# Performance work log

Hardware: AMD Instinct MI355X
Metric: run time of the kernel (lower is better)

The kernel has to match this reference:

```python
import jax, jax.numpy as jnp
import numpy as np

EXPANSION_RATES = [10, 25]
NEG_SLOPE = 0.2


def gat_layer(x_self, x_neigh, W, a_self, a_neigh):
    """Multi-head GAT attention over a fixed neighbor fanout.

    x_self:  [M, F]      target-node features
    x_neigh: [M, K, F]   K sampled neighbors per target
    W:       [H, F, D]   per-head projection
    a_self:  [H, D]      attention vector (self part)
    a_neigh: [H, D]      attention vector (neighbor part)
    returns  [M, H*D]    concatenated heads
    """
    hs = jnp.einsum('mf,hfd->mhd', x_self, W)              # [M,H,D]
    hn = jnp.einsum('mkf,hfd->mkhd', x_neigh, W)           # [M,K,H,D]
    e_self = jnp.einsum('mhd,hd->mh', hs, a_self)          # [M,H]
    e_neigh = jnp.einsum('mkhd,hd->mkh', hn, a_neigh)      # [M,K,H]
    e = jax.nn.leaky_relu(e_self[:, None, :] + e_neigh, NEG_SLOPE)
    alpha = jax.nn.softmax(e, axis=1)                      # softmax over K neighbors
    out = jnp.einsum('mkh,mkhd->mhd', alpha, hn)           # [M,H,D]
    return out.reshape(out.shape[0], -1)                   # concat heads


def setup_inputs() -> dict:
    key = jax.random.key(0)
    ks = jax.random.split(key, 10)
    B, F, D, H, OUT = 1024, 128, 128, 2, 128
    r0, r1 = EXPANSION_RATES
    inp = {}
    # hierarchical embeddings: level j has B * prod(rates[:j]) rows
    inp['h0'] = jax.random.normal(ks[0], (B, F), dtype=jnp.float32)
    inp['h1'] = jax.random.normal(ks[1], (B * r0, F), dtype=jnp.float32)
    inp['h2'] = jax.random.normal(ks[2], (B * r0 * r1, F), dtype=jnp.float32)
    # layer 0: consumes raw features (F); layer 1: consumes H*D
    inp['W0'] = jax.random.normal(ks[3], (H, F, D), dtype=jnp.float32) / np.sqrt(F)
    inp['a_self0'] = jax.random.normal(ks[4], (H, D), dtype=jnp.float32) / np.sqrt(D)
    inp['a_neigh0'] = jax.random.normal(ks[5], (H, D), dtype=jnp.float32) / np.sqrt(D)
    inp['W1'] = jax.random.normal(ks[6], (H, H * D, D), dtype=jnp.float32) / np.sqrt(H * D)
    inp['a_self1'] = jax.random.normal(ks[7], (H, D), dtype=jnp.float32) / np.sqrt(D)
    inp['a_neigh1'] = jax.random.normal(ks[8], (H, D), dtype=jnp.float32) / np.sqrt(D)
    inp['fc_W'] = jax.random.normal(ks[9], (H * D, OUT), dtype=jnp.float32) / np.sqrt(H * D)
    return inp


def reference(h0, h1, h2, W0, a_self0, a_neigh0, W1, a_self1, a_neigh1, fc_W):
    hidden = [h0, h1, h2]
    layers = [(W0, a_self0, a_neigh0), (W1, a_self1, a_neigh1)]
    depth = len(EXPANSION_RATES)
    for i, (W, a_s, a_n) in enumerate(layers):
        for j in range(depth - i):
            x_self = hidden[j]                                   # [M, F_i]
            M = x_self.shape[0]
            # neighbor rows of level j+1 grouped in blocks of expansion_rates[j]
            x_neigh = hidden[j + 1].reshape(M, EXPANSION_RATES[j], x_self.shape[1])
            hidden[j] = gat_layer(x_self, x_neigh, W, a_s, a_n)  # [M, H*D]
    return hidden[0] @ fc_W                                      # [B, OUT]
```

## Files before the change

### kernel.cpp

```cpp
#include <hip/hip_runtime.h>

#define LRELU_SLOPE 0.2f

#define OFF_UV0  0u
#define OFF_U1   512u
#define OFF_V1   1024u
#define OFF_P    1536u
#define OFF_PP   2048u
#define OFF_Q    4096u
#define OFF_R    69632u
#define OFF_Y1   135168u
#define OFF_Y0   2756608u

__device__ __forceinline__ float dot4(float4 a, float4 b) {
    return a.x * b.x + a.y * b.y + a.z * b.z + a.w * b.w;
}

template<int CTRL>
__device__ __forceinline__ float dppmov(float x) {
    return __int_as_float(__builtin_amdgcn_update_dpp(
        0, __float_as_int(x), CTRL, 0xf, 0xf, true));
}
__device__ __forceinline__ float sum16(float x) {
    x += dppmov<0xB1>(x);
    x += dppmov<0x4E>(x);
    x += dppmov<0x141>(x);
    x += dppmov<0x140>(x);
    return x;
}
__device__ __forceinline__ float sum32(float x) {
    x = sum16(x);
    return x + __shfl_xor(x, 16);
}
__device__ __forceinline__ float sum64(float x) {
    float y = sum32(x);
    return y + __shfl_xor(y, 32);
}
__device__ __forceinline__ float lrelu(float x) {
    return (x >= 0.f) ? x : LRELU_SLOPE * x;
}

__global__ __launch_bounds__(256)
void prepA_kernel(const float* __restrict__ W0, const float* __restrict__ as0,
                  const float* __restrict__ an0,
                  const float* __restrict__ W1, const float* __restrict__ as1,
                  const float* __restrict__ an1,
                  const float* __restrict__ fcW, float* __restrict__ ws) {
    __shared__ float s[16 * 129];
    const int b = blockIdx.x;
    const int t = threadIdx.x;
    if (b < 192) {
        const int wid = b * 4 + (t >> 6);
        const int lane = t & 63;
        const float *wrow, *as, *an;
        if (wid < 256) {
            wrow = W0 + (size_t)wid * 128;
            int h = wid >> 7;
            as = as0 + h * 128; an = an0 + h * 128;
        } else {
            int g = wid - 256;
            wrow = W1 + (size_t)g * 128;
            int h = g >> 8;
            as = as1 + h * 128; an = an1 + h * 128;
        }
        float2 w = *(const float2*)(wrow + 2 * lane);
        float2 sv = *(const float2*)(as + 2 * lane);
        float2 nv = *(const float2*)(an + 2 * lane);
        float au = sum64(w.x * sv.x + w.y * sv.y);
        float av = sum64(w.x * nv.x + w.y * nv.y);
        if (lane == 0) {
            if (wid < 256) { ws[OFF_UV0 + wid] = au; ws[OFF_UV0 + 256 + wid] = av; }
            else { int g = wid - 256; ws[OFF_U1 + g] = au; ws[OFF_V1 + g] = av; }
        }
    } else {
        const int idx = b - 192;
        const int h = idx >> 4, g0 = (idx & 15) * 16;
        const float* Wh = W1 + (size_t)h * 32768;
        for (int ii = t * 4; ii < 16 * 128; ii += 1024) {
            int i = ii >> 7, d = ii & 127;
            float4 g4 = *(const float4*)(Wh + (size_t)(g0 + i) * 128 + d);
            s[i * 129 + d + 0] = g4.x;
            s[i * 129 + d + 1] = g4.y;
            s[i * 129 + d + 2] = g4.z;
            s[i * 129 + d + 3] = g4.w;
        }
        __syncthreads();
        const int dg = t & 31, rg = t >> 5;
        float4 acc[2];
        acc[0] = make_float4(0.f, 0.f, 0.f, 0.f);
        acc[1] = make_float4(0.f, 0.f, 0.f, 0.f);
        const float* fp = fcW + (size_t)h * 16384 + 4 * dg;
        #pragma unroll 4
        for (int d2 = 0; d2 < 128; ++d2) {
            float4 f4 = *(const float4*)(fp + (size_t)d2 * 128);
            #pragma unroll
            for (int j = 0; j < 2; ++j) {
                float x = s[(rg * 2 + j) * 129 + d2];
                acc[j].x += x * f4.x; acc[j].y += x * f4.y;
                acc[j].z += x * f4.z; acc[j].w += x * f4.w;
            }
        }
        float* Qp = ws + OFF_Q + (size_t)h * 32768;
        #pragma unroll
        for (int j = 0; j < 2; ++j)
            *(float4*)(Qp + (size_t)(g0 + rg * 2 + j) * 128 + 4 * dg) = acc[j];
    }
}

__device__ __forceinline__ void upd2(float& m, float& s, float4& A,
                                     float ea, float eb,
                                     const float4& xa, const float4& xb) {
    float mn = fmaxf(m, fmaxf(ea, eb));
    float sc = __expf(m - mn);
    float pa = __expf(ea - mn);
    float pb = __expf(eb - mn);
    s = s * sc + pa + pb;
    A.x = A.x * sc + pa * xa.x + pb * xb.x;
    A.y = A.y * sc + pa * xa.y + pb * xb.y;
    A.z = A.z * sc + pa * xa.z + pb * xb.z;
    A.w = A.w * sc + pa * xa.w + pb * xb.w;
    m = mn;
}
__device__ __forceinline__ void upd1(float& m, float& s, float4& A,
                                     float ea, const float4& xa) {
    float mn = fmaxf(m, ea);
    float sc = __expf(m - mn);
    float pa = __expf(ea - mn);
    s = s * sc + pa;
    A.x = A.x * sc + pa * xa.x;
    A.y = A.y * sc + pa * xa.y;
    A.z = A.z * sc + pa * xa.z;
    A.w = A.w * sc + pa * xa.w;
    m = mn;
}

__global__ __launch_bounds__(256)
void big6_kernel(const float* __restrict__ h0, const float* __restrict__ h1,
                 const float* __restrict__ h2, const float* __restrict__ W0,
                 float* __restrict__ ws) {
    const int b = blockIdx.x;
    const int t = threadIdx.x;
    const float* uv0 = ws + OFF_UV0;

    if (b < 1280) {
        const int lane = t & 63;
        const int sub = lane >> 5;
        const int fl = lane & 31;
        const int m = (b * 4 + (t >> 6)) * 2 + sub;
        const float* xnp = h2 + (size_t)m * 3200;
        float es0, es1;
        {
            const float4 xs = *(const float4*)(h1 + (size_t)m * 128 + 4 * fl);
            const float4 u0 = *(const float4*)(uv0 + 0 + 4 * fl);
            const float4 u1 = *(const float4*)(uv0 + 128 + 4 * fl);
            es0 = sum32(dot4(xs, u0));
            es1 = sum32(dot4(xs, u1));
        }
        const float4 v0 = *(const float4*)(uv0 + 256 + 4 * fl);
        const float4 v1 = *(const float4*)(uv0 + 384 + 4 * fl);

        float4 xa = *(const float4*)(xnp + 4 * fl);
        float4 xb = *(const float4*)(xnp + 128 + 4 * fl);
        float4 xc = *(const float4*)(xnp + 256 + 4 * fl);
        float4 xd = *(const float4*)(xnp + 384 + 4 * fl);
        float m0 = -1e30f, m1 = -1e30f, s0 = 0.f, s1 = 0.f;
        float4 A0 = make_float4(0.f, 0.f, 0.f, 0.f);
        float4 A1 = make_float4(0.f, 0.f, 0.f, 0.f);
        #pragma unroll
        for (int c = 0; c < 12; ++c) {
            float4 na, nb;
            if (c < 10) {
                na = *(const float4*)(xnp + (size_t)(2 * c + 4) * 128 + 4 * fl);
                nb = *(const float4*)(xnp + (size_t)(2 * c + 5) * 128 + 4 * fl);
            } else if (c == 10) {
                na = *(const float4*)(xnp + (size_t)24 * 128 + 4 * fl);
                nb = na;
            } else {
                na = xc; nb = xd;
            }
            float ea0 = lrelu(es0 + sum32(dot4(xa, v0)));
            float ea1 = lrelu(es1 + sum32(dot4(xa, v1)));
            float eb0 = lrelu(es0 + sum32(dot4(xb, v0)));
            float eb1 = lrelu(es1 + sum32(dot4(xb, v1)));
            upd2(m0, s0, A0, ea0, eb0, xa, xb);
            upd2(m1, s1, A1, ea1, eb1, xa, xb);
            xa = xc; xb = xd; xc = na; xd = nb;
        }
        {
            float e0 = lrelu(es0 + sum32(dot4(xa, v0)));
            float e1 = lrelu(es1 + sum32(dot4(xa, v1)));
            upd1(m0, s0, A0, e0, xa);
            upd1(m1, s1, A1, e1, xa);
        }
        const float i0 = 1.f / s0, i1 = 1.f / s1;
        float4 o0, o1;
        o0.x = A0.x * i0; o0.y = A0.y * i0; o0.z = A0.z * i0; o0.w = A0.w * i0;
        o1.x = A1.x * i1; o1.y = A1.y * i1; o1.z = A1.z * i1; o1.w = A1.w * i1;
        *(float4*)(ws + OFF_Y1 + (size_t)m * 256 + 4 * fl) = o0;
        *(float4*)(ws + OFF_Y1 + (size_t)m * 256 + 128 + 4 * fl) = o1;
    } else if (b < 1408) {
        const int lane = t & 63;
        const int sub = lane >> 5;
        const int fl = lane & 31;
        const int m = ((b - 1280) * 4 + (t >> 6)) * 2 + sub;
        const float* xnp = h1 + (size_t)m * 1280;
        float es0, es1;
        {
            const float4 xs = *(const float4*)(h0 + (size_t)m * 128 + 4 * fl);
            const float4 u0 = *(const float4*)(uv0 + 0 + 4 * fl);
            const float4 u1 = *(const float4*)(uv0 + 128 + 4 * fl);
            es0 = sum32(dot4(xs, u0));
            es1 = sum32(dot4(xs, u1));
        }
        const float4 v0 = *(const float4*)(uv0 + 256 + 4 * fl);
        const float4 v1 = *(const float4*)(uv0 + 384 + 4 * fl);

        float4 xa = *(const float4*)(xnp + 4 * fl);
        float4 xb = *(const float4*)(xnp + 128 + 4 * fl);
        float4 xc = *(const float4*)(xnp + 256 + 4 * fl);
        float4 xd = *(const float4*)(xnp + 384 + 4 * fl);
        float m0 = -1e30f, m1 = -1e30f, s0 = 0.f, s1 = 0.f;
        float4 A0 = make_float4(0.f, 0.f, 0.f, 0.f);
        float4 A1 = make_float4(0.f, 0.f, 0.f, 0.f);
        #pragma unroll
        for (int c = 0; c < 5; ++c) {
            float4 na, nb;
            if (c < 3) {
                na = *(const float4*)(xnp + (size_t)(2 * c + 4) * 128 + 4 * fl);
                nb = *(const float4*)(xnp + (size_t)(2 * c + 5) * 128 + 4 * fl);
            } else {
                na = xc; nb = xd;
            }
            float ea0 = lrelu(es0 + sum32(dot4(xa, v0)));
            float ea1 = lrelu(es1 + sum32(dot4(xa, v1)));
            float eb0 = lrelu(es0 + sum32(dot4(xb, v0)));
            float eb1 = lrelu(es1 + sum32(dot4(xb, v1)));
            upd2(m0, s0, A0, ea0, eb0, xa, xb);
            upd2(m1, s1, A1, ea1, eb1, xa, xb);
            xa = xc; xb = xd; xc = na; xd = nb;
        }
        const float i0 = 1.f / s0, i1 = 1.f / s1;
        float4 o0, o1;
        o0.x = A0.x * i0; o0.y = A0.y * i0; o0.z = A0.z * i0; o0.w = A0.w * i0;
        o1.x = A1.x * i1; o1.y = A1.y * i1; o1.z = A1.z * i1; o1.w = A1.w * i1;
        *(float4*)(ws + OFF_Y0 + (size_t)m * 256 + 4 * fl) = o0;
        *(float4*)(ws + OFF_Y0 + (size_t)m * 256 + 128 + 4 * fl) = o1;
    } else if (b < 1536) {
        const int wid = (b - 1408) * 4 + (t >> 6);
        const int lane = t & 63;
        const int h = wid >> 8, rest = wid & 255;
        const int h0i = rest >> 7;
        const float* wrow = W0 + (size_t)rest * 128;
        float2 w2 = *(const float2*)(wrow + 2 * lane);
        float2 su = *(const float2*)(ws + OFF_U1 + h * 256 + h0i * 128 + 2 * lane);
        float2 sv = *(const float2*)(ws + OFF_V1 + h * 256 + h0i * 128 + 2 * lane);
        float pu = sum64(w2.x * su.x + w2.y * su.y);
        float pv = sum64(w2.x * sv.x + w2.y * sv.y);
        if (lane == 0) { ws[OFF_PP + wid] = pu; ws[OFF_P + wid] = pv; }
    } else {
        __shared__ float smem[2064];
        const int idx = b - 1536;
        const int h = idx >> 4;
        const int h0i = (idx >> 3) & 1;
        const int f0 = (idx & 7) * 16;
        const float* W0h = W0 + (size_t)h0i * 16384;
        for (int ii = t * 4; ii < 16 * 128; ii += 1024) {
            int i = ii >> 7, d = ii & 127;
            float4 g4 = *(const float4*)(W0h + (size_t)(f0 + i) * 128 + d);
            smem[i * 129 + d + 0] = g4.x;
            smem[i * 129 + d + 1] = g4.y;
            smem[i * 129 + d + 2] = g4.z;
            smem[i * 129 + d + 3] = g4.w;
        }
        __syncthreads();
        const int dg = t & 31, rg = t >> 5;
        float4 acc[2];
        acc[0] = make_float4(0.f, 0.f, 0.f, 0.f);
        acc[1] = make_float4(0.f, 0.f, 0.f, 0.f);
        const float* Qp = ws + OFF_Q + (size_t)h * 32768 + (size_t)h0i * 16384 + 4 * dg;
        #pragma unroll 4
        for (int d = 0; d < 128; ++d) {
            float4 q4 = *(const float4*)(Qp + (size_t)d * 128);
            #pragma unroll
            for (int j = 0; j < 2; ++j) {
                float x = smem[(rg * 2 + j) * 129 + d];
                acc[j].x += x * q4.x; acc[j].y += x * q4.y;
                acc[j].z += x * q4.z; acc[j].w += x * q4.w;
            }
        }
        float* Rp = ws + OFF_R + (size_t)h * 32768 + (size_t)h0i * 16384;
        #pragma unroll
        for (int j = 0; j < 2; ++j)
            *(float4*)(Rp + (size_t)(f0 + rg * 2 + j) * 128 + 4 * dg) = acc[j];
    }
}

__global__ __launch_bounds__(512)
void final_kernel(const float* __restrict__ ws, float* __restrict__ out) {
    __shared__ float xn[22 * 256];
    __shared__ float yb[1024];
    __shared__ float pr[8][2][128];
    __shared__ float en[2][11][2];
    __shared__ float al[2][10][2];
    const int t = threadIdx.x;
    const int m0 = blockIdx.x * 2;
    const int rlane = t & 63;
    const int rg = t >> 6;
    const float* P  = ws + OFF_P;
    const float* Pp = ws + OFF_PP;
    const float* Y1 = ws + OFF_Y1;
    const float* Y0 = ws + OFF_Y0;
    const float4 su0 = *(const float4*)(Pp + 0 + 4 * rlane);
    const float4 su1 = *(const float4*)(Pp + 256 + 4 * rlane);
    const float4 nv0 = *(const float4*)(P + 0 + 4 * rlane);
    const float4 nv1 = *(const float4*)(P + 256 + 4 * rlane);
    float4 g[3];
    #pragma unroll
    for (int i = 0; i < 3; ++i) {
        int rho = rg + 8 * i;
        if (rho < 22) {
            int r = rho / 11, k = rho % 11;
            int m = m0 + r;
            const float* src = (k < 10) ? (Y1 + ((size_t)m * 10 + k) * 256)
                                        : (Y0 + (size_t)m * 256);
            g[i] = *(const float4*)(src + 4 * rlane);
        }
    }
    #pragma unroll
    for (int i = 0; i < 3; ++i) {
        int rho = rg + 8 * i;
        if (rho < 22) {
            int r = rho / 11, k = rho % 11;
            *(float4*)(&xn[rho * 256 + 4 * rlane]) = g[i];
            float p0 = sum64(dot4(g[i], (k < 10) ? nv0 : su0));
            float p1 = sum64(dot4(g[i], (k < 10) ? nv1 : su1));
            if (rlane == 0) { en[r][k][0] = p0; en[r][k][1] = p1; }
        }
    }
    __syncthreads();
    if (t < 128) {
        int r = t >> 6, h = (t >> 5) & 1, k = t & 31;
        float e = -1e30f;
        if (k < 10) {
            float z = en[r][10][h] + en[r][k][h];
            e = (z >= 0.f) ? z : LRELU_SLOPE * z;
        }
        float mx = e;
        #pragma unroll
        for (int off = 16; off > 0; off >>= 1) mx = fmaxf(mx, __shfl_xor(mx, off));
        float ex = (k < 10) ? __expf(e - mx) : 0.f;
        float sm = ex;
        #pragma unroll
        for (int off = 16; off > 0; off >>= 1) sm += __shfl_xor(sm, off);
        if (k < 10) al[r][k][h] = ex / sm;
    }
    __syncthreads();
    #pragma unroll
    for (int i = 0; i < 2; ++i) {
        int c = t + 512 * i;
        int r = c >> 9, rem = c & 511, h = rem >> 8, f = rem & 255;
        float acc = 0.f;
        #pragma unroll
        for (int k = 0; k < 10; ++k) acc += al[r][k][h] * xn[(r * 11 + k) * 256 + f];
        yb[c] = acc;
    }
    __syncthreads();
    {
        const int seg = t >> 6;
        const int op = (t & 63) * 2;
        const float* Rv = ws + OFF_R + (size_t)seg * 64 * 128 + op;
        const float* y0p = yb + seg * 64;
        const float* y1p = yb + 512 + seg * 64;
        float2 a0 = make_float2(0.f, 0.f), a1 = make_float2(0.f, 0.f);
        #pragma unroll 8
        for (int gi = 0; gi < 64; ++gi) {
            float2 rv = *(const float2*)(Rv + (size_t)gi * 128);
            float ya = y0p[gi], yc = y1p[gi];
            a0.x += ya * rv.x; a0.y += ya * rv.y;
            a1.x += yc * rv.x; a1.y += yc * rv.y;
        }
        pr[seg][0][op] = a0.x; pr[seg][0][op + 1] = a0.y;
        pr[seg][1][op] = a1.x; pr[seg][1][op + 1] = a1.y;
    }
    __syncthreads();
    if (t < 256) {
        const int r = t >> 7, o = t & 127;
        float acc = 0.f;
        #pragma unroll
        for (int s = 0; s < 8; ++s) acc += pr[s][r][o];
        out[(size_t)(m0 + r) * 128 + o] = acc;
    }
}

extern "C" void kernel_launch(void* const* d_in, const int* in_sizes, int n_in,
                              void* d_out, int out_size, void* d_ws, size_t ws_size,
                              hipStream_t stream) {
    const float* h0  = (const float*)d_in[0];
    const float* h1  = (const float*)d_in[1];
    const float* h2  = (const float*)d_in[2];
    const float* W0  = (const float*)d_in[3];
    const float* as0 = (const float*)d_in[4];
    const float* an0 = (const float*)d_in[5];
    const float* W1  = (const float*)d_in[6];
    const float* as1 = (const float*)d_in[7];
    const float* an1 = (const float*)d_in[8];
    const float* fcW = (const float*)d_in[9];
    float* outp = (float*)d_out;
    float* ws = (float*)d_ws;

    hipLaunchKernelGGL(prepA_kernel, dim3(224), dim3(256), 0, stream,
                       W0, as0, an0, W1, as1, an1, fcW, ws);
    hipLaunchKernelGGL(big6_kernel, dim3(1568), dim3(256), 0, stream,
                       h0, h1, h2, W0, ws);
    hipLaunchKernelGGL(final_kernel, dim3(512), dim3(512), 0, stream,
                       ws, outp);
}
```

Before: 59.17 us.

## Stage neighbor rows into LDS via direct global-to-LDS loads, one target per wave

The level-1 attention path now gives each wave a single target node. It bulk-loads all 25 neighbor rows plus the self row straight into shared memory with global_load_lds, then waits once for all of them. The two half-waves each process alternating neighbor rows with an online softmax, and the partial states are merged across halves with shuffles. This replaces the register-prefetch pipeline over global loads and doubles the block count for that path. The cost is about 53 KB of LDS per block, which limits occupancy, and a full wait on the loads before any compute starts.

```diff
diff --git a/kernel.cpp b/kernel.cpp
--- a/kernel.cpp
+++ b/kernel.cpp
@@ -38,6 +38,15 @@
 }
 __device__ __forceinline__ float lrelu(float x) {
     return (x >= 0.f) ? x : LRELU_SLOPE * x;
+}
+
+__device__ __forceinline__ void glds16(const float* gsrc, float* ldst) {
+#if defined(__HIP_DEVICE_COMPILE__)
+    __builtin_amdgcn_global_load_lds(
+        (const __attribute__((address_space(1))) unsigned int*)gsrc,
+        (__attribute__((address_space(3))) unsigned int*)ldst,
+        16, 0, 0);
+#endif
 }
 
 __global__ __launch_bounds__(256)
@@ -135,74 +144,79 @@
 }
 
 __global__ __launch_bounds__(256)
-void big6_kernel(const float* __restrict__ h0, const float* __restrict__ h1,
+void big7_kernel(const float* __restrict__ h0, const float* __restrict__ h1,
                  const float* __restrict__ h2, const float* __restrict__ W0,
                  float* __restrict__ ws) {
+    __shared__ float xl[4 * 3328];
     const int b = blockIdx.x;
     const int t = threadIdx.x;
     const float* uv0 = ws + OFF_UV0;
 
-    if (b < 1280) {
+    if (b < 2560) {
+        const int w = t >> 6;
+        const int lane = t & 63;
+        const int half = lane >> 5;
+        const int fl = lane & 31;
+        const int m = b * 4 + w;
+        float* tb = xl + w * 3328;
+
+        {
+            const float* src = h2 + (size_t)m * 3200;
+            #pragma unroll
+            for (int i = 0; i < 12; ++i)
+                glds16(src + i * 256 + lane * 4, tb + i * 256);
+            const float* g12 = (lane < 32) ? (src + 3072 + lane * 4)
+                                           : (h1 + (size_t)m * 128 + (lane - 32) * 4);
+            glds16(g12, tb + 3072);
+            asm volatile("s_waitcnt vmcnt(0)" ::: "memory");
+        }
+
+        const float4 u0 = *(const float4*)(uv0 + 0 + 4 * fl);
+        const float4 u1 = *(const float4*)(uv0 + 128 + 4 * fl);
+        const float4 v0 = *(const float4*)(uv0 + 256 + 4 * fl);
+        const float4 v1 = *(const float4*)(uv0 + 384 + 4 * fl);
+        float es0, es1;
+        {
+            float4 xs = *(const float4*)(tb + 3200 + 4 * fl);
+            es0 = sum32(dot4(xs, u0));
+            es1 = sum32(dot4(xs, u1));
+        }
+        float m0 = -1e30f, m1 = -1e30f, s0 = 0.f, s1 = 0.f;
+        float4 A0 = make_float4(0.f, 0.f, 0.f, 0.f);
+        float4 A1 = make_float4(0.f, 0.f, 0.f, 0.f);
+        #pragma unroll
+        for (int i = 0; i < 13; ++i) {
+            int row = 2 * i + half;
+            const bool dead = (row > 24);
+            if (dead) row = 24;
+            float4 x = *(const float4*)(tb + row * 128 + 4 * fl);
+            float e0 = lrelu(es0 + sum32(dot4(x, v0)));
+            float e1 = lrelu(es1 + sum32(dot4(x, v1)));
+            if (dead) { e0 = -1e30f; e1 = -1e30f; }
+            upd1(m0, s0, A0, e0, x);
+            upd1(m1, s1, A1, e1, x);
+        }
+        float g0 = fmaxf(m0, __shfl_xor(m0, 32));
+        float g1 = fmaxf(m1, __shfl_xor(m1, 32));
+        float c0 = __expf(m0 - g0), c1 = __expf(m1 - g1);
+        s0 *= c0; s1 *= c1;
+        A0.x *= c0; A0.y *= c0; A0.z *= c0; A0.w *= c0;
+        A1.x *= c1; A1.y *= c1; A1.z *= c1; A1.w *= c1;
+        s0 += __shfl_xor(s0, 32); s1 += __shfl_xor(s1, 32);
+        A0.x += __shfl_xor(A0.x, 32); A0.y += __shfl_xor(A0.y, 32);
+        A0.z += __shfl_xor(A0.z, 32); A0.w += __shfl_xor(A0.w, 32);
+        A1.x += __shfl_xor(A1.x, 32); A1.y += __shfl_xor(A1.y, 32);
+        A1.z += __shfl_xor(A1.z, 32); A1.w += __shfl_xor(A1.w, 32);
+        const float inv = 1.f / (half ? s1 : s0);
+        const float4 S = half ? A1 : A0;
+        float4 o;
+        o.x = S.x * inv; o.y = S.y * inv; o.z = S.z * inv; o.w = S.w * inv;
+        *(float4*)(ws + OFF_Y1 + (size_t)m * 256 + half * 128 + 4 * fl) = o;
+    } else if (b < 2688) {
         const int lane = t & 63;
         const int sub = lane >> 5;
         const int fl = lane & 31;
-        const int m = (b * 4 + (t >> 6)) * 2 + sub;
-        const float* xnp = h2 + (size_t)m * 3200;
-        float es0, es1;
-        {
-            const float4 xs = *(const float4*)(h1 + (size_t)m * 128 + 4 * fl);
-            const float4 u0 = *(const float4*)(uv0 + 0 + 4 * fl);
-            const float4 u1 = *(const float4*)(uv0 + 128 + 4 * fl);
-            es0 = sum32(dot4(xs, u0));
-            es1 = sum32(dot4(xs, u1));
-        }
-        const float4 v0 = *(const float4*)(uv0 + 256 + 4 * fl);
-        const float4 v1 = *(const float4*)(uv0 + 384 + 4 * fl);
-
-        float4 xa = *(const float4*)(xnp + 4 * fl);
-        float4 xb = *(const float4*)(xnp + 128 + 4 * fl);
-        float4 xc = *(const float4*)(xnp + 256 + 4 * fl);
-        float4 xd = *(const float4*)(xnp + 384 + 4 * fl);
-        float m0 = -1e30f, m1 = -1e30f, s0 = 0.f, s1 = 0.f;
-        float4 A0 = make_float4(0.f, 0.f, 0.f, 0.f);
-        float4 A1 = make_float4(0.f, 0.f, 0.f, 0.f);
-        #pragma unroll
-        for (int c = 0; c < 12; ++c) {
-            float4 na, nb;
-            if (c < 10) {
-                na = *(const float4*)(xnp + (size_t)(2 * c + 4) * 128 + 4 * fl);
-                nb = *(const float4*)(xnp + (size_t)(2 * c + 5) * 128 + 4 * fl);
-            } else if (c == 10) {
-                na = *(const float4*)(xnp + (size_t)24 * 128 + 4 * fl);
-                nb = na;
-            } else {
-                na = xc; nb = xd;
-            }
-            float ea0 = lrelu(es0 + sum32(dot4(xa, v0)));
-            float ea1 = lrelu(es1 + sum32(dot4(xa, v1)));
-            float eb0 = lrelu(es0 + sum32(dot4(xb, v0)));
-            float eb1 = lrelu(es1 + sum32(dot4(xb, v1)));
-            upd2(m0, s0, A0, ea0, eb0, xa, xb);
-            upd2(m1, s1, A1, ea1, eb1, xa, xb);
-            xa = xc; xb = xd; xc = na; xd = nb;
-        }
-        {
-            float e0 = lrelu(es0 + sum32(dot4(xa, v0)));
-            float e1 = lrelu(es1 + sum32(dot4(xa, v1)));
-            upd1(m0, s0, A0, e0, xa);
-            upd1(m1, s1, A1, e1, xa);
-        }
-        const float i0 = 1.f / s0, i1 = 1.f / s1;
-        float4 o0, o1;
-        o0.x = A0.x * i0; o0.y = A0.y * i0; o0.z = A0.z * i0; o0.w = A0.w * i0;
-        o1.x = A1.x * i1; o1.y = A1.y * i1; o1.z = A1.z * i1; o1.w = A1.w * i1;
-        *(float4*)(ws + OFF_Y1 + (size_t)m * 256 + 4 * fl) = o0;
-        *(float4*)(ws + OFF_Y1 + (size_t)m * 256 + 128 + 4 * fl) = o1;
-    } else if (b < 1408) {
-        const int lane = t & 63;
-        const int sub = lane >> 5;
-        const int fl = lane & 31;
-        const int m = ((b - 1280) * 4 + (t >> 6)) * 2 + sub;
+        const int m = ((b - 2560) * 4 + (t >> 6)) * 2 + sub;
         const float* xnp = h1 + (size_t)m * 1280;
         float es0, es1;
         {
@@ -245,8 +259,8 @@
         o1.x = A1.x * i1; o1.y = A1.y * i1; o1.z = A1.z * i1; o1.w = A1.w * i1;
         *(float4*)(ws + OFF_Y0 + (size_t)m * 256 + 4 * fl) = o0;
         *(float4*)(ws + OFF_Y0 + (size_t)m * 256 + 128 + 4 * fl) = o1;
-    } else if (b < 1536) {
-        const int wid = (b - 1408) * 4 + (t >> 6);
+    } else if (b < 2816) {
+        const int wid = (b - 2688) * 4 + (t >> 6);
         const int lane = t & 63;
         const int h = wid >> 8, rest = wid & 255;
         const int h0i = rest >> 7;
@@ -258,8 +272,8 @@
         float pv = sum64(w2.x * sv.x + w2.y * sv.y);
         if (lane == 0) { ws[OFF_PP + wid] = pu; ws[OFF_P + wid] = pv; }
     } else {
-        __shared__ float smem[2064];
-        const int idx = b - 1536;
+        float* smem = xl;
+        const int idx = b - 2816;
         const int h = idx >> 4;
         const int h0i = (idx >> 3) & 1;
         const int f0 = (idx & 7) * 16;
@@ -410,7 +424,7 @@
 
     hipLaunchKernelGGL(prepA_kernel, dim3(224), dim3(256), 0, stream,
                        W0, as0, an0, W1, as1, an1, fcW, ws);
-    hipLaunchKernelGGL(big6_kernel, dim3(1568), dim3(256), 0, stream,
+    hipLaunchKernelGGL(big7_kernel, dim3(2848), dim3(256), 0, stream,
                        h0, h1, h2, W0, ws);
     hipLaunchKernelGGL(final_kernel, dim3(512), dim3(512), 0, stream,
                        ws, outp);
```

New measurement: 64.45 us. 8.9% more time.

## Process four targets per block in final kernel and drop neighbor smem staging

Applied to the files above, without the earlier changes.

The final kernel now handles four target rows per block instead of two, halving the grid so each block's reads of the R matrix are reused across four rows. The shared-memory copy of neighbor features is removed; the attention-weighted sum reads Y1 from global memory a second time, relying on cache hits. This lowers LDS use and R traffic per row, in exchange for a repeated global read of Y1 and fewer blocks to spread across the GPU.

```diff
diff --git a/kernel.cpp b/kernel.cpp
--- a/kernel.cpp
+++ b/kernel.cpp
@@ -296,14 +296,13 @@
 }
 
 __global__ __launch_bounds__(512)
-void final_kernel(const float* __restrict__ ws, float* __restrict__ out) {
-    __shared__ float xn[22 * 256];
-    __shared__ float yb[1024];
-    __shared__ float pr[8][2][128];
-    __shared__ float en[2][11][2];
-    __shared__ float al[2][10][2];
+void final4_kernel(const float* __restrict__ ws, float* __restrict__ out) {
+    __shared__ float yb[2048];
+    __shared__ float pr[8][4][128];
+    __shared__ float en[4][11][2];
+    __shared__ float al[4][10][2];
     const int t = threadIdx.x;
-    const int m0 = blockIdx.x * 2;
+    const int m0 = blockIdx.x * 4;
     const int rlane = t & 63;
     const int rg = t >> 6;
     const float* P  = ws + OFF_P;
@@ -314,31 +313,23 @@
     const float4 su1 = *(const float4*)(Pp + 256 + 4 * rlane);
     const float4 nv0 = *(const float4*)(P + 0 + 4 * rlane);
     const float4 nv1 = *(const float4*)(P + 256 + 4 * rlane);
-    float4 g[3];
+
     #pragma unroll
-    for (int i = 0; i < 3; ++i) {
+    for (int i = 0; i < 6; ++i) {
         int rho = rg + 8 * i;
-        if (rho < 22) {
+        if (rho < 44) {
             int r = rho / 11, k = rho % 11;
             int m = m0 + r;
             const float* src = (k < 10) ? (Y1 + ((size_t)m * 10 + k) * 256)
                                         : (Y0 + (size_t)m * 256);
-            g[i] = *(const float4*)(src + 4 * rlane);
-        }
-    }
-    #pragma unroll
-    for (int i = 0; i < 3; ++i) {
-        int rho = rg + 8 * i;
-        if (rho < 22) {
-            int r = rho / 11, k = rho % 11;
-            *(float4*)(&xn[rho * 256 + 4 * rlane]) = g[i];
-            float p0 = sum64(dot4(g[i], (k < 10) ? nv0 : su0));
-            float p1 = sum64(dot4(g[i], (k < 10) ? nv1 : su1));
+            float4 g = *(const float4*)(src + 4 * rlane);
+            float p0 = sum64(dot4(g, (k < 10) ? nv0 : su0));
+            float p1 = sum64(dot4(g, (k < 10) ? nv1 : su1));
             if (rlane == 0) { en[r][k][0] = p0; en[r][k][1] = p1; }
         }
     }
     __syncthreads();
-    if (t < 128) {
+    if (t < 256) {
         int r = t >> 6, h = (t >> 5) & 1, k = t & 31;
         float e = -1e30f;
         if (k < 10) {
@@ -356,12 +347,13 @@
     }
     __syncthreads();
     #pragma unroll
-    for (int i = 0; i < 2; ++i) {
+    for (int i = 0; i < 4; ++i) {
         int c = t + 512 * i;
         int r = c >> 9, rem = c & 511, h = rem >> 8, f = rem & 255;
+        const float* base = Y1 + ((size_t)(m0 + r) * 10) * 256 + f;
         float acc = 0.f;
         #pragma unroll
-        for (int k = 0; k < 10; ++k) acc += al[r][k][h] * xn[(r * 11 + k) * 256 + f];
+        for (int k = 0; k < 10; ++k) acc += al[r][k][h] * base[k * 256];
         yb[c] = acc;
     }
     __syncthreads();
@@ -369,21 +361,27 @@
         const int seg = t >> 6;
         const int op = (t & 63) * 2;
         const float* Rv = ws + OFF_R + (size_t)seg * 64 * 128 + op;
-        const float* y0p = yb + seg * 64;
-        const float* y1p = yb + 512 + seg * 64;
-        float2 a0 = make_float2(0.f, 0.f), a1 = make_float2(0.f, 0.f);
-        #pragma unroll 8
+        float2 a[4];
+        #pragma unroll
+        for (int r = 0; r < 4; ++r) a[r] = make_float2(0.f, 0.f);
+        #pragma unroll 4
         for (int gi = 0; gi < 64; ++gi) {
             float2 rv = *(const float2*)(Rv + (size_t)gi * 128);
-            float ya = y0p[gi], yc = y1p[gi];
-            a0.x += ya * rv.x; a0.y += ya * rv.y;
-            a1.x += yc * rv.x; a1.y += yc * rv.y;
-        }
-        pr[seg][0][op] = a0.x; pr[seg][0][op + 1] = a0.y;
-        pr[seg][1][op] = a1.x; pr[seg][1][op + 1] = a1.y;
+            #pragma unroll
+            for (int r = 0; r < 4; ++r) {
+                float yv = yb[r * 512 + seg * 64 + gi];
+                a[r].x += yv * rv.x;
+                a[r].y += yv * rv.y;
+            }
+        }
+        #pragma unroll
+        for (int r = 0; r < 4; ++r) {
+            pr[seg][r][op] = a[r].x;
+            pr[seg][r][op + 1] = a[r].y;
+        }
     }
     __syncthreads();
-    if (t < 256) {
+    {
         const int r = t >> 7, o = t & 127;
         float acc = 0.f;
         #pragma unroll
@@ -412,6 +410,6 @@
                        W0, as0, an0, W1, as1, an1, fcW, ws);
     hipLaunchKernelGGL(big6_kernel, dim3(1568), dim3(256), 0, stream,
                        h0, h1, h2, W0, ws);
-    hipLaunchKernelGGL(final_kernel, dim3(512), dim3(512), 0, stream,
+    hipLaunchKernelGGL(final4_kernel, dim3(256), dim3(512), 0, stream,
                        ws, outp);
 }
```

Result: no change. 58.70 us (-0.8%).
